# Kernel tuning notes

Hardware: AMD Instinct MI355X
Metric: run time of the kernel (lower is better)

## Reference

```python
import jax, jax.numpy as jnp
import numpy as np
from jax import lax

H = 12  # num_heads (from init_kwargs)


def _orthogonal_landmarks(q, num_landmarks):
    # q: (B, N, D) already scaled. Faithful to torch loop: recursively pick the
    # point whose max |cos sim| to the already-selected landmarks is minimal.
    B, N, D = q.shape
    nrm = jnp.linalg.norm(q, axis=-1, keepdims=True)
    qk = q / jnp.maximum(nrm, 1e-12)
    bidx = jnp.arange(B)
    key = jax.random.key(42)
    idx0 = jax.random.randint(key, (B,), 0, N)
    cur = qk[bidx, idx0]                             # (B, D)
    # running max |cos sim|; selected rows pinned to 10 (as in torch code)
    max_sim = jnp.zeros((B, N), qk.dtype).at[bidx, idx0].set(10.0)

    def step(carry, _):
        max_sim, cur = carry
        cos = jnp.abs(jnp.einsum('bnd,bd->bn', qk, cur))
        max_sim = jnp.maximum(max_sim, cos)
        idx = jnp.argmin(max_sim, axis=-1)
        cur2 = qk[bidx, idx]
        max_sim = max_sim.at[bidx, idx].set(10.0)
        return (max_sim, cur2), idx

    (_, _), idxs = lax.scan(step, (max_sim, cur), None, length=num_landmarks - 1)
    all_idx = jnp.concatenate([idx0[None, :], idxs], axis=0).T  # (B, L)
    landmarks = q[bidx[:, None], all_idx]                        # unnormalized q rows
    return lax.stop_gradient(landmarks)


def _orthoformer(q, k, v, num_landmarks, num_frames):
    # q,k,v: (B*h, N, D);  N = F * P
    Bh, N, D = q.shape
    F = num_frames
    P = N // F
    sc = D ** (-0.25)
    q = q * sc
    k = k * sc
    lm = _orthogonal_landmarks(q, num_landmarks)                 # (Bh, L, D)
    kernel_1 = jax.nn.softmax(jnp.einsum('bnd,bld->bnl', q, lm), axis=-1)   # (Bh,N,L)
    k2 = jnp.einsum('bld,bnd->bln', lm, k).reshape(Bh, num_landmarks, F, P)
    kernel_2 = jax.nn.softmax(k2, axis=-1)                       # (Bh,L,F,P)
    vr = v.reshape(Bh, F, P, D)
    x = jnp.einsum('blfp,bfpd->blfd', kernel_2, vr)
    x = jnp.einsum('bnl,blfd->bnfd', kernel_1, x)                # (Bh,N,F,D)
    return x


def setup_inputs() -> dict:
    key = jax.random.key(0)
    ks = jax.random.split(key, 6)
    B, F, P, C = 2, 16, 196, 768
    N = F * P
    s = 0.02
    x = jax.random.normal(ks[0], (B, N, C), jnp.float32)
    W_qkv = jax.random.normal(ks[1], (C, 3 * C), jnp.float32) * s
    W_pq = jax.random.normal(ks[2], (C, C), jnp.float32) * s
    W_pkv = jax.random.normal(ks[3], (C, 2 * C), jnp.float32) * s
    W_proj = jax.random.normal(ks[4], (C, C), jnp.float32) * s
    b_proj = jnp.zeros((C,), jnp.float32)
    return {"x": x, "W_qkv": W_qkv, "W_pq": W_pq, "W_pkv": W_pkv,
            "W_proj": W_proj, "b_proj": b_proj,
            "seq_len": P, "num_frames": F, "num_landmarks": 128}


def reference(x, W_qkv, W_pq, W_pkv, W_proj, b_proj, seq_len, num_frames, num_landmarks):
    B, N, C = x.shape
    F, P, h = num_frames, seq_len, H
    d = C // h
    scale = d ** (-0.5)
    qkv = x @ W_qkv                                              # (B,N,3C)
    q, k, v = jnp.split(qkv, 3, axis=-1)
    def to_bh(t):  # b n (h d) -> (b h) n d
        return t.reshape(B, N, h, d).transpose(0, 2, 1, 3).reshape(B * h, N, d)
    q_, k_, v_ = to_bh(q), to_bh(k), to_bh(v)
    xo = _orthoformer(q_, k_, v_, num_landmarks, F)              # (B*h,N,F,d)
    # (b h) s f d -> b s f (h d)
    xo = xo.reshape(B, h, N, F, d).transpose(0, 2, 3, 1, 4).reshape(B, N, F, C)
    # diagonal over (frame-of-query g, frame-of-key f)
    xd = xo.reshape(B, F, P, F, C)
    xdiag = jnp.diagonal(xd, axis1=1, axis2=3)                   # (B,P,C,F)
    xdiag = jnp.moveaxis(xdiag, -1, 1).reshape(B, N, C)          # b (f p) d
    q2 = xdiag @ W_pq                                            # (B,N,C)
    k2, v2 = jnp.split(xo @ W_pkv, 2, axis=-1)                   # (B,N,F,C) each
    q2 = q2.reshape(B, N, h, d).transpose(0, 2, 1, 3) * scale    # (B,h,N,d)
    k2 = k2.reshape(B, N, F, h, d).transpose(0, 3, 1, 2, 4)      # (B,h,N,F,d)
    v2 = v2.reshape(B, N, F, h, d).transpose(0, 3, 1, 2, 4)
    attn = jax.nn.softmax(jnp.einsum('bhsd,bhsfd->bhsf', q2, k2), axis=-1)
    out = jnp.einsum('bhsf,bhsfd->bhsd', attn, v2)               # (B,h,N,d)
    out = out.transpose(0, 2, 1, 3).reshape(B, N, C)
    out = out @ W_proj + b_proj
    return out, attn
```

## Files before the change

### kernel.cpp

```cpp
#include <hip/hip_runtime.h>


using u16 = unsigned short;
using u32 = unsigned int;
using u64 = unsigned long long;

typedef short bf16x8 __attribute__((ext_vector_type(8)));
typedef float f32x4 __attribute__((ext_vector_type(4)));

#define N_ 3136
#define C_ 768
#define H_ 12
#define F_ 16
#define P_ 196
#define L_ 128
#define SC_ 0.35355339059327373f
#define OUTPART_ ((size_t)2 * N_ * C_)
#define KB_ 8
#define RPB_ 392

__device__ __forceinline__ float b2f(u16 u) {
  u32 x = ((u32)u) << 16; float f; __builtin_memcpy(&f, &x, 4); return f;
}
__device__ __forceinline__ float lo16f(u32 u) {
  u32 x = u << 16; float f; __builtin_memcpy(&f, &x, 4); return f;
}
__device__ __forceinline__ float hi16f(u32 u) {
  u32 x = u & 0xFFFF0000u; float f; __builtin_memcpy(&f, &x, 4); return f;
}
__device__ __forceinline__ u16 f2b(float f) {
  u32 u; __builtin_memcpy(&u, &f, 4);
  u32 r = (u + 0x7FFFu + ((u >> 16) & 1u)) >> 16;
  return (u16)r;
}
__device__ __forceinline__ u64 d2u(double d) { u64 u; __builtin_memcpy(&u, &d, 8); return u; }

__device__ __forceinline__ void gll16(const void* g, void* l) {
  __builtin_amdgcn_global_load_lds(
      (__attribute__((address_space(1))) void*)g,
      (__attribute__((address_space(3))) void*)l, 16, 0, 0);
}

__global__ void detect_k(const u32* __restrict__ w, int* __restrict__ flag) {
  const int t = threadIdx.x;
  int hits = 0;
  #pragma unroll
  for (int i = 0; i < 16; ++i) {
    u32 word = w[t * 16 + i];
    u32 e = (word >> 7) & 0xFFu;
    if (e >= 110u && e <= 126u) hits++;
  }
  #pragma unroll
  for (int off = 32; off > 0; off >>= 1) hits += __shfl_down(hits, off);
  if (t == 0) flag[0] = (hits >= 512) ? 0 : 1;
}

__global__ void zcnt_k(u64* __restrict__ p) { if (threadIdx.x < 384) p[threadIdx.x] = 0ull; }

__device__ __forceinline__ void tf2(u32 k0, u32 k1v, u32 c0, u32 c1, u32& o0, u32& o1) {
  u32 ks[3] = {k0, k1v, k0 ^ k1v ^ 0x1BD11BDAu};
  u32 x0 = c0 + ks[0], x1 = c1 + ks[1];
  const u32 rA[4] = {13u, 15u, 26u, 6u}, rB[4] = {17u, 29u, 16u, 24u};
  #pragma unroll
  for (int r = 0; r < 5; ++r) {
    #pragma unroll
    for (int q = 0; q < 4; ++q) {
      u32 rot = (r & 1) ? rB[q] : rA[q];
      x0 += x1; x1 = (x1 << rot) | (x1 >> (32u - rot)); x1 ^= x0;
    }
    x0 += ks[(r + 1) % 3];
    x1 += ks[(r + 2) % 3] + (u32)(r + 1);
  }
  o0 = x0; o1 = x1;
}

__device__ __forceinline__ int tf_idx0(int bh) {
  u32 a0, a1, b0, b1;
  tf2(0u, 42u, 0u, 0u, a0, a1);
  tf2(0u, 42u, 0u, 1u, b0, b1);
  u32 j = (u32)bh;
  u32 h0, h1, l0, l1;
  tf2(a0, a1, 0u, j, h0, h1);
  u32 hi = h0 ^ h1;
  tf2(b0, b1, 0u, j, l0, l1);
  u32 lo = l0 ^ l1;
  return (int)(((hi % 3136u) * 2048u + (lo % 3136u)) % 3136u);
}

__global__ __launch_bounds__(256) void qselT_k(const void* __restrict__ xr, const void* __restrict__ wr,
                                               const int* __restrict__ flagp, float* __restrict__ qt)
{
  __shared__ float As[64 * 20];
  __shared__ float Bs[16 * 64];
  const int t = threadIdx.x;
  const int m0 = blockIdx.x * 64;
  const int n0 = blockIdx.y * 64;
  const int f32i = flagp[0];
  const int tx = t & 15, ty = t >> 4;
  float acc[4][4];
  #pragma unroll
  for (int i = 0; i < 4; ++i)
    #pragma unroll
    for (int j = 0; j < 4; ++j) acc[i][j] = 0.f;

  const int alr = t >> 2;
  const int alk = (t & 3) * 4;
  const int bkr = t >> 4;
  const int bnc = (t & 15) * 4;

  for (int k0 = 0; k0 < 768; k0 += 16) {
    float4 av, bv;
    if (f32i) {
      av = *(const float4*)((const float*)xr + (size_t)(m0 + alr) * 768 + k0 + alk);
      bv = *(const float4*)((const float*)wr + (size_t)(k0 + bkr) * 2304 + n0 + bnc);
    } else {
      const u16* xa = (const u16*)xr + (size_t)(m0 + alr) * 768 + k0 + alk;
      const u16* wa = (const u16*)wr + (size_t)(k0 + bkr) * 2304 + n0 + bnc;
      av.x = b2f(xa[0]); av.y = b2f(xa[1]); av.z = b2f(xa[2]); av.w = b2f(xa[3]);
      bv.x = b2f(wa[0]); bv.y = b2f(wa[1]); bv.z = b2f(wa[2]); bv.w = b2f(wa[3]);
    }
    As[alr * 20 + alk + 0] = av.x; As[alr * 20 + alk + 1] = av.y;
    As[alr * 20 + alk + 2] = av.z; As[alr * 20 + alk + 3] = av.w;
    *(float4*)(&Bs[bkr * 64 + bnc]) = bv;
    __syncthreads();
    #pragma unroll
    for (int kk = 0; kk < 16; ++kk) {
      float a[4], b[4];
      #pragma unroll
      for (int i = 0; i < 4; ++i) a[i] = As[(ty * 4 + i) * 20 + kk];
      #pragma unroll
      for (int j = 0; j < 4; ++j) b[j] = Bs[kk * 64 + tx * 4 + j];
      #pragma unroll
      for (int i = 0; i < 4; ++i)
        #pragma unroll
        for (int j = 0; j < 4; ++j) acc[i][j] += a[i] * b[j];
    }
    __syncthreads();
  }
  #pragma unroll
  for (int i = 0; i < 4; ++i) {
    const int m = m0 + ty * 4 + i;
    const int b = m / N_, n = m - b * N_;
    #pragma unroll
    for (int j = 0; j < 4; ++j) {
      const int col = n0 + tx * 4 + j;
      const int hh = col >> 6, dd = col & 63;
      qt[((size_t)(b * H_ + hh) * 64 + dd) * N_ + n] = acc[i][j] * SC_;
    }
  }
}

__global__ __launch_bounds__(512, 1) void landmarksR_k(
    const float* __restrict__ qt, float* __restrict__ lm, u64* __restrict__ cand)
{
  const int kb = blockIdx.x;
  const int bh = blockIdx.y;
  const float* QT = qt + (size_t)bh * 64 * N_;
  float* LM = lm + (size_t)bh * L_ * 64;
  u64* cd = cand + (size_t)bh * 16;
  __shared__ double curD[64];
  __shared__ u64 redV[8];
  __shared__ int redI[8];
  __shared__ int sW;
  const int t = threadIdx.x;
  const bool act = (t < RPB_);
  const int g = t >> 2, dc = t & 3, d0 = dc * 16;
  const int r0 = kb * RPB_;
  const int myRow = r0 + t;
  const float* base = QT + r0 + 4 * g;

  float4 qreg[16];
  #pragma unroll
  for (int i = 0; i < 16; ++i) qreg[i] = (float4){0.f, 0.f, 0.f, 0.f};
  if (act) {
    #pragma unroll
    for (int i = 0; i < 16; ++i) qreg[i] = *(const float4*)(base + (size_t)(d0 + i) * N_);
  }

  double inv_own = 0.0, ms_own = 0.0;
  if (act) {
    double s0 = 0.0, s1 = 0.0, s2 = 0.0, s3 = 0.0;
    #pragma unroll
    for (int i = 0; i < 16; ++i) {
      const float4 v = qreg[i];
      s0 += (double)v.x * (double)v.x; s1 += (double)v.y * (double)v.y;
      s2 += (double)v.z * (double)v.z; s3 += (double)v.w * (double)v.w;
    }
    s0 += __shfl_xor(s0, 1); s1 += __shfl_xor(s1, 1);
    s2 += __shfl_xor(s2, 1); s3 += __shfl_xor(s3, 1);
    s0 += __shfl_xor(s0, 2); s1 += __shfl_xor(s1, 2);
    s2 += __shfl_xor(s2, 2); s3 += __shfl_xor(s3, 2);
    const double sown = (dc == 0) ? s0 : (dc == 1) ? s1 : (dc == 2) ? s2 : s3;
    inv_own = 1.0 / fmax(sqrt(sown), 1e-12);
  }
  const int idx0 = tf_idx0(bh);
  if (act && myRow == idx0) ms_own = 10.0;

  if (t < 64) {
    const float vf = QT[(size_t)t * N_ + idx0];
    double v = (double)vf;
    double s = v * v;
    #pragma unroll
    for (int off = 32; off; off >>= 1) s += __shfl_xor(s, off);
    curD[t] = v / fmax(sqrt(s), 1e-12);
    if (kb == 0) LM[t] = vf;
  }
  __syncthreads();

  for (int step = 1; step < 128; ++step) {
    u64 bV = d2u(1e30); int bI = 0x7fffffff;
    if (act) {
      double a0 = 0.0, a1 = 0.0, a2 = 0.0, a3 = 0.0;
      #pragma unroll
      for (int i = 0; i < 16; ++i) {
        const float4 v = qreg[i];
        const double c = curD[d0 + i];
        a0 += (double)v.x * c; a1 += (double)v.y * c;
        a2 += (double)v.z * c; a3 += (double)v.w * c;
      }
      a0 += __shfl_xor(a0, 1); a1 += __shfl_xor(a1, 1);
      a2 += __shfl_xor(a2, 1); a3 += __shfl_xor(a3, 1);
      a0 += __shfl_xor(a0, 2); a1 += __shfl_xor(a1, 2);
      a2 += __shfl_xor(a2, 2); a3 += __shfl_xor(a3, 2);
      const double aown = (dc == 0) ? a0 : (dc == 1) ? a1 : (dc == 2) ? a2 : a3;
      ms_own = fmax(ms_own, fabs(aown * inv_own));
      bV = d2u(ms_own); bI = myRow;
    }
    #pragma unroll
    for (int off = 32; off; off >>= 1) {
      const u64 ov = __shfl_xor(bV, off);
      const int oi = __shfl_xor(bI, off);
      if (ov < bV || (ov == bV && oi < bI)) { bV = ov; bI = oi; }
    }
    if ((t & 63) == 0) { redV[t >> 6] = bV; redI[t >> 6] = bI; }
    __syncthreads();
    const int par = step & 1;
    if (t == 0) {
      u64 v = redV[0]; int ix = redI[0];
      #pragma unroll
      for (int w2 = 1; w2 < 8; ++w2)
        if (redV[w2] < v || (redV[w2] == v && redI[w2] < ix)) { v = redV[w2]; ix = redI[w2]; }
      const u64 pk = (v & ~((1ull << 19) - 1ull)) | ((u64)(u32)(step & 127) << 12) | (u64)(u32)ix;
      __hip_atomic_store(&cd[par * KB_ + kb], pk, __ATOMIC_RELAXED, __HIP_MEMORY_SCOPE_AGENT);
    }
    if (t < 64) {
      u64 pv = ~0ull;
      int ok = 1;
      for (;;) {
        if (t < KB_) {
          pv = __hip_atomic_load(&cd[par * KB_ + t], __ATOMIC_RELAXED, __HIP_MEMORY_SCOPE_AGENT);
          ok = ((int)((pv >> 12) & 127u) == step) ? 1 : 0;
        }
        if (__all(ok)) break;
        __builtin_amdgcn_s_sleep(1);
      }
      u64 m = (t < KB_) ? pv : ~0ull;
      #pragma unroll
      for (int off = 1; off < KB_; off <<= 1) {
        const u64 o = __shfl_xor(m, off);
        if (o < m) m = o;
      }
      if (t == 0) sW = (int)(m & 0xFFFu);
    }
    __syncthreads();
    const int w = sW;
    if (act && myRow == w) ms_own = 10.0;
    if (t < 64) {
      const float vf = QT[(size_t)t * N_ + w];
      double v = (double)vf;
      double s = v * v;
      #pragma unroll
      for (int off = 32; off; off >>= 1) s += __shfl_xor(s, off);
      curD[t] = v / fmax(sqrt(s), 1e-12);
      if (kb == 0) LM[(size_t)step * 64 + t] = vf;
    }
    __syncthreads();
  }
}

__global__ __launch_bounds__(256) void twT_k(const void* __restrict__ W, int K, int Nn,
                                             const int* __restrict__ flagp, u16* __restrict__ WT)
{
  __shared__ u16 Ts[64][80];
  const int t = threadIdx.x;
  const int k0 = blockIdx.x * 64, n0 = blockIdx.y * 64;
  const int f32i = flagp[0];
  const int kr = t >> 2, nc = (t & 3) * 16;
  u16 tmp[16];
  if (f32i) {
    const float* p = (const float*)W + (size_t)(k0 + kr) * Nn + n0 + nc;
    #pragma unroll
    for (int j = 0; j < 16; ++j) tmp[j] = f2b(p[j]);
  } else {
    const u16* p = (const u16*)W + (size_t)(k0 + kr) * Nn + n0 + nc;
    #pragma unroll
    for (int j = 0; j < 16; ++j) tmp[j] = p[j];
  }
  #pragma unroll
  for (int j = 0; j < 16; ++j) Ts[kr][nc + j] = tmp[j];
  __syncthreads();
  const int nr = t >> 2, kc = (t & 3) * 16;
  u16 o[16];
  #pragma unroll
  for (int j = 0; j < 16; ++j) o[j] = Ts[kc + j][nr];
  u16* dst = WT + (size_t)(n0 + nr) * K + k0 + kc;
  *(uint4*)(dst) = *(uint4*)(o);
  *(uint4*)(dst + 8) = *(uint4*)(o + 8);
}

__global__ __launch_bounds__(256) void xcvt_k(const void* __restrict__ x,
                                              const int* __restrict__ flagp, u16* __restrict__ xb)
{
  const int i = blockIdx.x * 256 + threadIdx.x;
  if (flagp[0]) {
    const float4* p = (const float4*)x + (size_t)i * 2;
    float4 f0 = p[0], f1 = p[1];
    u16 tmp[8] = { f2b(f0.x), f2b(f0.y), f2b(f0.z), f2b(f0.w),
                   f2b(f1.x), f2b(f1.y), f2b(f1.z), f2b(f1.w) };
    *(uint4*)(xb + (size_t)i * 8) = *(uint4*)tmp;
  } else {
    ((uint4*)xb)[i] = ((const uint4*)x)[i];
  }
}

template <int MODE>
__global__ __launch_bounds__(256) void gemm_k(
    const void* __restrict__ Ap, const void* __restrict__ Bp,
    int M, int K, int lda, int ldb, int n0c, int cn, const int* __restrict__ flagp,
    float* __restrict__ of0, u16* __restrict__ ob0, u16* __restrict__ ob1, u16* __restrict__ ob2,
    const void* __restrict__ biasRaw, void* __restrict__ outRaw)
{
  __shared__ u16 As[128 * 32];
  __shared__ u16 Bs[128 * 32];
  const int t = threadIdx.x;
  const int m0 = blockIdx.x * 128;
  const int n0 = blockIdx.y * 128;
  const int rf = (MODE == 4) ? flagp[0] : 0;

  size_t aOff = 0, bOff = 0;
  if constexpr (MODE == 1) {
    const int bh = blockIdx.z;
    aOff = (size_t)bh * ((size_t)N_ * 128) + (size_t)n0c * 128;
    bOff = (size_t)bh * (1024 * 128);
  }
  const int lane = t & 63;
  const int w = t >> 6;
  const int mw = (w >> 1) * 64;
  const int nw = (w & 1) * 64;
  const int lr = lane & 15;
  const int lk = lane >> 4;

  f32x4 acc[4][4];
  #pragma unroll
  for (int i = 0; i < 4; ++i)
    #pragma unroll
    for (int j = 0; j < 4; ++j) acc[i][j] = (f32x4){0.f, 0.f, 0.f, 0.f};

  const int c0 = w * 2, c1 = c0 + 1;
  const int rl = lane >> 2, sl = lane & 3;
  const int rowA0 = c0 * 16 + rl, rowA1 = c1 * 16 + rl;
  const int segA0 = (sl ^ ((rowA0 ^ (rowA0 >> 2)) & 3)) * 8;
  const int segA1 = (sl ^ ((rowA1 ^ (rowA1 >> 2)) & 3)) * 8;
  int ga0 = m0 + rowA0; if (ga0 >= M) ga0 = M - 1;
  int ga1 = m0 + rowA1; if (ga1 >= M) ga1 = M - 1;
  const u16* A16 = (const u16*)Ap;
  const u16* B16 = (const u16*)Bp;
  const u16* aP0 = A16 + aOff + (size_t)ga0 * lda + segA0;
  const u16* aP1 = A16 + aOff + (size_t)ga1 * lda + segA1;
  const u16* bP0 = B16 + bOff + (size_t)(n0 + rowA0) * ldb + segA0;
  const u16* bP1 = B16 + bOff + (size_t)(n0 + rowA1) * ldb + segA1;
  u16* lA0 = &As[c0 * 512]; u16* lA1 = &As[c1 * 512];
  u16* lB0 = &Bs[c0 * 512]; u16* lB1 = &Bs[c1 * 512];

  int roA[4], roB[4];
  #pragma unroll
  for (int q = 0; q < 4; ++q) {
    const int ra = mw + q * 16 + lr;
    roA[q] = ra * 32 + ((lk ^ ((ra ^ (ra >> 2)) & 3)) * 8);
    const int rb = nw + q * 16 + lr;
    roB[q] = rb * 32 + ((lk ^ ((rb ^ (rb >> 2)) & 3)) * 8);
  }

  for (int k0 = 0; k0 < K; k0 += 32) {
    gll16(aP0 + k0, lA0);
    gll16(aP1 + k0, lA1);
    gll16(bP0 + k0, lB0);
    gll16(bP1 + k0, lB1);
    __syncthreads();

    bf16x8 af[4], bfv[4];
    #pragma unroll
    for (int mt = 0; mt < 4; ++mt) af[mt] = *(const bf16x8*)(&As[roA[mt]]);
    #pragma unroll
    for (int nt = 0; nt < 4; ++nt) bfv[nt] = *(const bf16x8*)(&Bs[roB[nt]]);
    #pragma unroll
    for (int mt = 0; mt < 4; ++mt)
      #pragma unroll
      for (int nt = 0; nt < 4; ++nt)
        acc[mt][nt] = __builtin_amdgcn_mfma_f32_16x16x32_bf16(af[mt], bfv[nt], acc[mt][nt], 0, 0, 0);
    __syncthreads();
  }

  #pragma unroll
  for (int mt = 0; mt < 4; ++mt) {
    #pragma unroll
    for (int nt = 0; nt < 4; ++nt) {
      #pragma unroll
      for (int r = 0; r < 4; ++r) {
        const int grow = m0 + mw + mt * 16 + lk * 4 + r;
        const int gcol = n0 + nw + nt * 16 + lr;
        if (grow >= M) continue;
        float vv = acc[mt][nt][r];
        if constexpr (MODE == 0) {
          int b = (grow >= N_) ? 1 : 0;
          int n = grow - b * N_;
          int t3 = gcol / C_, cc = gcol - t3 * C_;
          int hh = cc >> 6, dd = cc & 63;
          size_t dst = (((size_t)(b * H_ + hh)) * N_ + n) * 64 + dd;
          if (t3 == 0) ob0[dst] = f2b(vv * SC_);
          else if (t3 == 1) ob1[dst] = f2b(vv * SC_);
          else ob2[dst] = f2b(vv);
        } else if constexpr (MODE == 1) {
          const int bh = blockIdx.z;
          int b = bh / H_, hh = bh - b * H_;
          int f = gcol >> 6, dd = gcol & 63;
          u16 wv = f2b(vv);
          ob0[(((size_t)(b * cn + grow)) * F_ + f) * C_ + hh * 64 + dd] = wv;
          int n = n0c + grow;
          if (f == n / P_) ob1[((size_t)(b * cn + grow)) * C_ + hh * 64 + dd] = wv;
        } else if constexpr (MODE == 2) {
          const int cn16 = cn * F_;
          int b = (grow >= cn16) ? 1 : 0;
          int r2 = grow - b * cn16;
          int ln = r2 >> 4, f = r2 & 15;
          int t2 = (gcol >= C_) ? 1 : 0, cc = gcol - t2 * C_;
          int hh = cc >> 6, dd = cc & 63;
          size_t dst = ((((size_t)(b * H_ + hh)) * cn + ln) * F_ + f) * 64 + dd;
          if (t2) ob1[dst] = f2b(vv); else ob0[dst] = f2b(vv);
        } else if constexpr (MODE == 3) {
          int b = (grow >= cn) ? 1 : 0;
          int ln = grow - b * cn;
          int hh = gcol >> 6, dd = gcol & 63;
          of0[(((size_t)(b * H_ + hh)) * cn + ln) * 64 + dd] = vv * 0.125f;
        } else {
          float bvad = rf ? ((const float*)biasRaw)[gcol] : b2f(((const u16*)biasRaw)[gcol]);
          float ov = vv + bvad;
          if (rf) ((float*)outRaw)[(size_t)grow * C_ + gcol] = ov;
          else    ((u16*)outRaw)[(size_t)grow * C_ + gcol] = f2b(ov);
        }
      }
    }
  }
}

__global__ __launch_bounds__(256) void k1_k(const u16* __restrict__ qb,
                                            const float* __restrict__ lm,
                                            u16* __restrict__ k1)
{
  const int bh = blockIdx.y;
  const int r0 = blockIdx.x * 64;
  __shared__ float qT[64][65];
  __shared__ float lmS[128 * 64];
  __shared__ float redA[4][64];
  __shared__ float redB[64];
  const int t = threadIdx.x;
  const u16* Q = qb + ((size_t)bh * N_ + r0) * 64;
  const float* Lm = lm + (size_t)bh * L_ * 64;
  for (int u = t; u < 2048; u += 256) ((float4*)lmS)[u] = ((const float4*)Lm)[u];
  for (int u = t; u < 512; u += 256) {
    int row = u >> 3, j0 = (u & 7) * 8;
    uint4 pk = *(const uint4*)(Q + (size_t)row * 64 + j0);
    const u16* pu = (const u16*)&pk;
    #pragma unroll
    for (int jj = 0; jj < 8; ++jj) qT[j0 + jj][row] = b2f(pu[jj]);
  }
  __syncthreads();
  const int row = t & 63, ch = t >> 6;
  float qr[64];
  #pragma unroll
  for (int j = 0; j < 64; ++j) qr[j] = qT[j][row];
  float s[32];
  for (int li = 0; li < 32; ++li) {
    const float* lp = lmS + (ch * 32 + li) * 64;
    float a = 0.f;
    #pragma unroll
    for (int j = 0; j < 64; ++j) a += lp[j] * qr[j];
    s[li] = a;
  }
  float mx = -1e30f;
  for (int li = 0; li < 32; ++li) mx = fmaxf(mx, s[li]);
  redA[ch][row] = mx;
  __syncthreads();
  if (t < 64) redB[t] = fmaxf(fmaxf(redA[0][t], redA[1][t]), fmaxf(redA[2][t], redA[3][t]));
  __syncthreads();
  mx = redB[row];
  float sum = 0.f;
  for (int li = 0; li < 32; ++li) { float e = __expf(s[li] - mx); s[li] = e; sum += e; }
  __syncthreads();
  redA[ch][row] = sum;
  __syncthreads();
  if (t < 64) redB[t] = 1.0f / (redA[0][t] + redA[1][t] + redA[2][t] + redA[3][t]);
  __syncthreads();
  const float inv = redB[row];
  u16* out = k1 + ((size_t)bh * N_ + r0 + row) * 128 + ch * 32;
  for (int li = 0; li < 32; ++li) out[li] = f2b(s[li] * inv);
}

__global__ __launch_bounds__(256) void k2x1_k(const float* __restrict__ lm,
                                              const u16* __restrict__ kb,
                                              const u16* __restrict__ vb,
                                              u16* __restrict__ x1)
{
  const int bh = blockIdx.x;
  const int f = blockIdx.y;
  __shared__ u16 kS[P_ * 64];
  __shared__ u16 vS[P_ * 64];
  __shared__ float redM[2][128];
  __shared__ float redS[2][128];
  const int t = threadIdx.x;
  const u16* Kf = kb + ((size_t)bh * N_ + f * P_) * 64;
  const u16* Vf = vb + ((size_t)bh * N_ + f * P_) * 64;
  for (int u = t; u < 1568; u += 256) {
    ((uint4*)kS)[u] = ((const uint4*)Kf)[u];
    ((uint4*)vS)[u] = ((const uint4*)Vf)[u];
  }
  __syncthreads();
  const int l = t & 127, half = t >> 7;
  const float* lp = lm + ((size_t)bh * L_ + l) * 64;
  float lr[64];
  #pragma unroll
  for (int j = 0; j < 64; ++j) lr[j] = lp[j];

  const int p0 = half * 98, p1 = p0 + 98;
  float mx = -1e30f;
  for (int p = p0; p < p1; ++p) {
    const uint4* kp = (const uint4*)(kS + p * 64);
    float s = 0.f;
    #pragma unroll
    for (int q4 = 0; q4 < 8; ++q4) {
      uint4 pk = kp[q4];
      const u32* pu = (const u32*)&pk;
      #pragma unroll
      for (int j2 = 0; j2 < 4; ++j2) {
        u32 u = pu[j2];
        s += lr[q4 * 8 + j2 * 2] * lo16f(u) + lr[q4 * 8 + j2 * 2 + 1] * hi16f(u);
      }
    }
    mx = fmaxf(mx, s);
  }
  redM[half][l] = mx;
  __syncthreads();
  mx = fmaxf(redM[0][l], redM[1][l]);

  float sm = 0.f;
  for (int p = p0; p < p1; ++p) {
    const uint4* kp = (const uint4*)(kS + p * 64);
    float s = 0.f;
    #pragma unroll
    for (int q4 = 0; q4 < 8; ++q4) {
      uint4 pk = kp[q4];
      const u32* pu = (const u32*)&pk;
      #pragma unroll
      for (int j2 = 0; j2 < 4; ++j2) {
        u32 u = pu[j2];
        s += lr[q4 * 8 + j2 * 2] * lo16f(u) + lr[q4 * 8 + j2 * 2 + 1] * hi16f(u);
      }
    }
    sm += __expf(s - mx);
  }
  redS[half][l] = sm;
  __syncthreads();
  const float inv = 1.0f / (redS[0][l] + redS[1][l]);

  const int dd0 = half * 32;
  float acc[32];
  #pragma unroll
  for (int u = 0; u < 32; ++u) acc[u] = 0.f;
  for (int p = 0; p < P_; ++p) {
    const uint4* kp = (const uint4*)(kS + p * 64);
    float s = 0.f;
    #pragma unroll
    for (int q4 = 0; q4 < 8; ++q4) {
      uint4 pk = kp[q4];
      const u32* pu = (const u32*)&pk;
      #pragma unroll
      for (int j2 = 0; j2 < 4; ++j2) {
        u32 u = pu[j2];
        s += lr[q4 * 8 + j2 * 2] * lo16f(u) + lr[q4 * 8 + j2 * 2 + 1] * hi16f(u);
      }
    }
    const float e = __expf(s - mx);
    const uint4* vp = (const uint4*)(vS + p * 64 + dd0);
    #pragma unroll
    for (int q4 = 0; q4 < 4; ++q4) {
      uint4 pv = vp[q4];
      const u32* pu = (const u32*)&pv;
      #pragma unroll
      for (int j2 = 0; j2 < 4; ++j2) {
        u32 u = pu[j2];
        acc[q4 * 8 + j2 * 2]     += e * lo16f(u);
        acc[q4 * 8 + j2 * 2 + 1] += e * hi16f(u);
      }
    }
  }
  u16* outT = x1 + (size_t)bh * (1024 * 128) + (size_t)(f * 64 + dd0) * 128 + l;
  for (int u = 0; u < 32; ++u) outT[(size_t)u * 128] = f2b(acc[u] * inv);
}

__global__ __launch_bounds__(256) void attn_k(const float* __restrict__ q2c,
                                              const u16* __restrict__ k2c,
                                              const u16* __restrict__ v2c,
                                              int n0c, int cn, const int* __restrict__ flagp,
                                              void* __restrict__ outRaw,
                                              u16* __restrict__ o)
{
  const int bh = blockIdx.y;
  const int b = bh / H_, hh = bh - b * H_;
  const int t = threadIdx.x;
  const int f32o = flagp[0];
  __shared__ float aS[64][17];
  const int nl = t >> 2, qi = t & 3;
  const int ln = blockIdx.x * 64 + nl;
  const bool act = ln < cn;
  const int n = n0c + ln;
  float q[64];
  if (act) {
    const float* qr = q2c + ((size_t)bh * cn + ln) * 64;
    #pragma unroll
    for (int j = 0; j < 64; ++j) q[j] = qr[j];
    float lg[4];
    #pragma unroll
    for (int ff = 0; ff < 4; ++ff) {
      const int f = qi * 4 + ff;
      const u16* kp = k2c + (((size_t)bh * cn + ln) * F_ + f) * 64;
      float s = 0.f;
      #pragma unroll
      for (int j8 = 0; j8 < 8; ++j8) {
        uint4 pk = ((const uint4*)kp)[j8];
        const u16* pu = (const u16*)&pk;
        #pragma unroll
        for (int u = 0; u < 8; ++u) s += q[j8 * 8 + u] * b2f(pu[u]);
      }
      lg[ff] = s;
    }
    float mx = fmaxf(fmaxf(lg[0], lg[1]), fmaxf(lg[2], lg[3]));
    mx = fmaxf(mx, __shfl_xor(mx, 1));
    mx = fmaxf(mx, __shfl_xor(mx, 2));
    float e[4], sm = 0.f;
    #pragma unroll
    for (int ff = 0; ff < 4; ++ff) { e[ff] = __expf(lg[ff] - mx); sm += e[ff]; }
    sm += __shfl_xor(sm, 1);
    sm += __shfl_xor(sm, 2);
    const float iv = 1.0f / sm;
    const size_t abase = ((size_t)bh * N_ + n) * F_ + qi * 4;
    #pragma unroll
    for (int ff = 0; ff < 4; ++ff) {
      const float a = e[ff] * iv;
      if (f32o) ((float*)outRaw)[OUTPART_ + abase + ff] = a;
      else      ((u16*)outRaw)[OUTPART_ + abase + ff] = f2b(a);
      aS[nl][qi * 4 + ff] = a;
    }
  }
  __syncthreads();
  if (act) {
    const int dd0 = qi * 16;
    float acc[16];
    #pragma unroll
    for (int u = 0; u < 16; ++u) acc[u] = 0.f;
    for (int f = 0; f < F_; ++f) {
      const float w2 = aS[nl][f];
      const u16* vp = v2c + (((size_t)bh * cn + ln) * F_ + f) * 64 + dd0;
      uint4 pv0 = ((const uint4*)vp)[0], pv1 = ((const uint4*)vp)[1];
      const u16* pu0 = (const u16*)&pv0;
      const u16* pu1 = (const u16*)&pv1;
      #pragma unroll
      for (int u = 0; u < 8; ++u) acc[u] += w2 * b2f(pu0[u]);
      #pragma unroll
      for (int u = 0; u < 8; ++u) acc[8 + u] += w2 * b2f(pu1[u]);
    }
    u16* op = o + ((size_t)(b * N_ + n)) * C_ + hh * 64 + dd0;
    for (int u = 0; u < 16; ++u) op[u] = f2b(acc[u]);
  }
}

extern "C" void kernel_launch(void* const* d_in, const int* in_sizes, int n_in,
                              void* d_out, int out_size, void* d_ws, size_t ws_size,
                              hipStream_t stream)
{
  (void)in_sizes; (void)n_in; (void)out_size;
  const void* x     = d_in[0];
  const void* Wqkv  = d_in[1];
  const void* Wpq   = d_in[2];
  const void* Wpkv  = d_in[3];
  const void* Wproj = d_in[4];
  const void* bproj = d_in[5];

  char* ws = (char*)d_ws;
  size_t off = 0;
  auto alloc = [&](size_t bytes) { void* p = ws + off; off += (bytes + 255) & ~(size_t)255; return p; };
  int*  flagp = (int*)alloc(256);
  u16*  qb  = (u16*)alloc(9633792);
  u16*  kb  = (u16*)alloc(9633792);
  u16*  vb  = (u16*)alloc(9633792);
  float* lm = (float*)alloc(786432);
  u16*  x1b = (u16*)alloc(6291456);
  u16*  ob  = (u16*)alloc(9633792);
  const size_t k1off = off;
  u16*  k1b = (u16*)alloc(19267584);
  const size_t chunk0 = off;

  const size_t qtNeed = k1off + 19267584 + 256;

  int Nc = 0;
  {
    const int cands[5] = {3136, 1568, 784, 392, 196};
    for (int i = 0; i < 5; ++i) {
      size_t need = chunk0 + (size_t)156672 * cands[i] + 1024;
      if (need <= ws_size && qtNeed <= ws_size) { Nc = cands[i]; break; }
    }
  }
  if (Nc == 0) return;
  const int nchunks = N_ / Nc;
  u16*  xoc = (u16*)(ws + chunk0);
  u16*  k2c = xoc + (size_t)24576 * Nc;
  u16*  v2c = k2c + (size_t)24576 * Nc;
  u16*  xdc = v2c + (size_t)24576 * Nc;
  float* q2c = (float*)(xdc + (size_t)1536 * Nc);
  float* qt  = (float*)(ws + k1off);

  u16* WqkvT = (u16*)(ws + k1off);
  u16* xb    = (u16*)(ws + k1off + 3538944);
  u16* WpkvT = kb;
  u16* WpqT  = kb + 1179648;
  u16* WprojT= kb + 1179648 + 589824;

  u64* cand = (u64*)(ws + chunk0);

  detect_k<<<1, 64, 0, stream>>>((const u32*)Wqkv, flagp);
  zcnt_k<<<1, 512, 0, stream>>>(cand);

  qselT_k<<<dim3(98, 12), 256, 0, stream>>>(x, Wqkv, flagp, qt);
  landmarksR_k<<<dim3(KB_, 24), 512, 0, stream>>>(qt, lm, cand);

  twT_k<<<dim3(12, 36), 256, 0, stream>>>(Wqkv, 768, 2304, flagp, WqkvT);
  xcvt_k<<<2352, 256, 0, stream>>>(x, flagp, xb);

  gemm_k<0><<<dim3(49, 18, 1), 256, 0, stream>>>(xb, WqkvT, 6272, 768, 768, 768, 0, 0, flagp,
                                                 nullptr, qb, kb, vb, nullptr, nullptr);
  k2x1_k<<<dim3(24, 16), 256, 0, stream>>>(lm, kb, vb, x1b);
  k1_k<<<dim3(49, 24), 256, 0, stream>>>(qb, lm, k1b);

  twT_k<<<dim3(12, 24), 256, 0, stream>>>(Wpkv, 768, 1536, flagp, WpkvT);
  twT_k<<<dim3(12, 12), 256, 0, stream>>>(Wpq, 768, 768, flagp, WpqT);
  twT_k<<<dim3(12, 12), 256, 0, stream>>>(Wproj, 768, 768, flagp, WprojT);

  for (int c = 0; c < nchunks; ++c) {
    const int n0c = c * Nc;
    gemm_k<1><<<dim3((Nc + 127) / 128, 8, 24), 256, 0, stream>>>(
        k1b, x1b, Nc, 128, 128, 128, n0c, Nc, flagp, nullptr, xoc, xdc, nullptr, nullptr, nullptr);
    gemm_k<2><<<dim3((2 * Nc * 16) / 128, 12, 1), 256, 0, stream>>>(
        xoc, WpkvT, 2 * Nc * 16, 768, 768, 768, n0c, Nc, flagp, nullptr, k2c, v2c, nullptr, nullptr, nullptr);
    gemm_k<3><<<dim3((2 * Nc + 127) / 128, 6, 1), 256, 0, stream>>>(
        xdc, WpqT, 2 * Nc, 768, 768, 768, n0c, Nc, flagp, q2c, nullptr, nullptr, nullptr, nullptr, nullptr);
    attn_k<<<dim3((Nc + 63) / 64, 24), 256, 0, stream>>>(
        q2c, k2c, v2c, n0c, Nc, flagp, d_out, ob);
  }
  gemm_k<4><<<dim3(49, 6, 1), 256, 0, stream>>>(ob, WprojT, 6272, 768, 768, 768, 0, 0, flagp,
                                                nullptr, nullptr, nullptr, nullptr, bproj, d_out);
}
```

Measured before the change: 1.770 ms.

## Merge weight transposes and post-projection GEMMs into fewer launches, retile qsel

Measured after the change: 1.658 ms. 6.3% less time.

```diff
diff --git a/kernel.cpp b/kernel.cpp
--- a/kernel.cpp
+++ b/kernel.cpp
@@ -90,56 +90,62 @@
 __global__ __launch_bounds__(256) void qselT_k(const void* __restrict__ xr, const void* __restrict__ wr,
                                                const int* __restrict__ flagp, float* __restrict__ qt)
 {
-  __shared__ float As[64 * 20];
+  __shared__ float As[128 * 20];
   __shared__ float Bs[16 * 64];
   const int t = threadIdx.x;
-  const int m0 = blockIdx.x * 64;
+  const int m0 = blockIdx.x * 128;
   const int n0 = blockIdx.y * 64;
   const int f32i = flagp[0];
   const int tx = t & 15, ty = t >> 4;
-  float acc[4][4];
-  #pragma unroll
-  for (int i = 0; i < 4; ++i)
+  float acc[8][4];
+  #pragma unroll
+  for (int i = 0; i < 8; ++i)
     #pragma unroll
     for (int j = 0; j < 4; ++j) acc[i][j] = 0.f;
 
-  const int alr = t >> 2;
-  const int alk = (t & 3) * 4;
+  const int alr = t >> 1;
+  const int alk = (t & 1) * 8;
   const int bkr = t >> 4;
   const int bnc = (t & 15) * 4;
 
   for (int k0 = 0; k0 < 768; k0 += 16) {
-    float4 av, bv;
+    float av[8];
+    float4 bv;
     if (f32i) {
-      av = *(const float4*)((const float*)xr + (size_t)(m0 + alr) * 768 + k0 + alk);
+      const float* xa = (const float*)xr + (size_t)(m0 + alr) * 768 + k0 + alk;
+      float4 a0 = *(const float4*)(xa);
+      float4 a1 = *(const float4*)(xa + 4);
+      av[0] = a0.x; av[1] = a0.y; av[2] = a0.z; av[3] = a0.w;
+      av[4] = a1.x; av[5] = a1.y; av[6] = a1.z; av[7] = a1.w;
       bv = *(const float4*)((const float*)wr + (size_t)(k0 + bkr) * 2304 + n0 + bnc);
     } else {
       const u16* xa = (const u16*)xr + (size_t)(m0 + alr) * 768 + k0 + alk;
+      #pragma unroll
+      for (int j = 0; j < 8; ++j) av[j] = b2f(xa[j]);
       const u16* wa = (const u16*)wr + (size_t)(k0 + bkr) * 2304 + n0 + bnc;
-      av.x = b2f(xa[0]); av.y = b2f(xa[1]); av.z = b2f(xa[2]); av.w = b2f(xa[3]);
       bv.x = b2f(wa[0]); bv.y = b2f(wa[1]); bv.z = b2f(wa[2]); bv.w = b2f(wa[3]);
     }
-    As[alr * 20 + alk + 0] = av.x; As[alr * 20 + alk + 1] = av.y;
-    As[alr * 20 + alk + 2] = av.z; As[alr * 20 + alk + 3] = av.w;
+    #pragma unroll
+    for (int j = 0; j < 8; ++j) As[alr * 20 + alk + j] = av[j];
     *(float4*)(&Bs[bkr * 64 + bnc]) = bv;
     __syncthreads();
     #pragma unroll
     for (int kk = 0; kk < 16; ++kk) {
-      float a[4], b[4];
-      #pragma unroll
-      for (int i = 0; i < 4; ++i) a[i] = As[(ty * 4 + i) * 20 + kk];
+      float a[8], b[4];
+      #pragma unroll
+      for (int i = 0; i < 8; ++i) a[i] = As[(ty * 8 + i) * 20 + kk];
       #pragma unroll
       for (int j = 0; j < 4; ++j) b[j] = Bs[kk * 64 + tx * 4 + j];
       #pragma unroll
-      for (int i = 0; i < 4; ++i)
+      for (int i = 0; i < 8; ++i)
         #pragma unroll
         for (int j = 0; j < 4; ++j) acc[i][j] += a[i] * b[j];
     }
     __syncthreads();
   }
   #pragma unroll
-  for (int i = 0; i < 4; ++i) {
-    const int m = m0 + ty * 4 + i;
+  for (int i = 0; i < 8; ++i) {
+    const int m = m0 + ty * 8 + i;
     const int b = m / N_, n = m - b * N_;
     #pragma unroll
     for (int j = 0; j < 4; ++j) {
@@ -153,8 +159,8 @@
 __global__ __launch_bounds__(512, 1) void landmarksR_k(
     const float* __restrict__ qt, float* __restrict__ lm, u64* __restrict__ cand)
 {
-  const int kb = blockIdx.x;
-  const int bh = blockIdx.y;
+  const int kb = blockIdx.y;
+  const int bh = blockIdx.x;
   const float* QT = qt + (size_t)bh * 64 * N_;
   float* LM = lm + (size_t)bh * L_ * 64;
   u64* cd = cand + (size_t)bh * 16;
@@ -278,13 +284,9 @@
   }
 }
 
-__global__ __launch_bounds__(256) void twT_k(const void* __restrict__ W, int K, int Nn,
-                                             const int* __restrict__ flagp, u16* __restrict__ WT)
-{
-  __shared__ u16 Ts[64][80];
-  const int t = threadIdx.x;
-  const int k0 = blockIdx.x * 64, n0 = blockIdx.y * 64;
-  const int f32i = flagp[0];
+__device__ __forceinline__ void twT_body(const void* W, int K, int Nn, int f32i,
+                                         u16* WT, int k0, int n0, int t, u16 (&Ts)[64][80])
+{
   const int kr = t >> 2, nc = (t & 3) * 16;
   u16 tmp[16];
   if (f32i) {
@@ -306,6 +308,26 @@
   u16* dst = WT + (size_t)(n0 + nr) * K + k0 + kc;
   *(uint4*)(dst) = *(uint4*)(o);
   *(uint4*)(dst + 8) = *(uint4*)(o + 8);
+}
+
+__global__ __launch_bounds__(256) void twT_k(const void* __restrict__ W, int K, int Nn,
+                                             const int* __restrict__ flagp, u16* __restrict__ WT)
+{
+  __shared__ u16 Ts[64][80];
+  twT_body(W, K, Nn, flagp[0], WT, blockIdx.x * 64, blockIdx.y * 64, threadIdx.x, Ts);
+}
+
+__global__ __launch_bounds__(256) void twT3_k(const void* __restrict__ W0, const void* __restrict__ W1,
+                                              const void* __restrict__ W2, const int* __restrict__ flagp,
+                                              u16* __restrict__ T0, u16* __restrict__ T1, u16* __restrict__ T2)
+{
+  __shared__ u16 Ts[64][80];
+  const int z = blockIdx.z;
+  const void* W = (z == 0) ? W0 : (z == 1) ? W1 : W2;
+  u16* WT = (z == 0) ? T0 : (z == 1) ? T1 : T2;
+  const int Nn = (z == 0) ? 1536 : 768;
+  if (blockIdx.y * 64 >= Nn) return;
+  twT_body(W, 768, Nn, flagp[0], WT, blockIdx.x * 64, blockIdx.y * 64, threadIdx.x, Ts);
 }
 
 __global__ __launch_bounds__(256) void xcvt_k(const void* __restrict__ x,
@@ -323,39 +345,23 @@
   }
 }
 
-template <int MODE>
-__global__ __launch_bounds__(256) void gemm_k(
-    const void* __restrict__ Ap, const void* __restrict__ Bp,
-    int M, int K, int lda, int ldb, int n0c, int cn, const int* __restrict__ flagp,
-    float* __restrict__ of0, u16* __restrict__ ob0, u16* __restrict__ ob1, u16* __restrict__ ob2,
-    const void* __restrict__ biasRaw, void* __restrict__ outRaw)
-{
-  __shared__ u16 As[128 * 32];
-  __shared__ u16 Bs[128 * 32];
-  const int t = threadIdx.x;
-  const int m0 = blockIdx.x * 128;
-  const int n0 = blockIdx.y * 128;
-  const int rf = (MODE == 4) ? flagp[0] : 0;
-
-  size_t aOff = 0, bOff = 0;
-  if constexpr (MODE == 1) {
-    const int bh = blockIdx.z;
-    aOff = (size_t)bh * ((size_t)N_ * 128) + (size_t)n0c * 128;
-    bOff = (size_t)bh * (1024 * 128);
-  }
+struct GemmCore {
+  const u16 *aP0, *aP1, *bP0, *bP1;
+  u16 *lA0, *lA1, *lB0, *lB1;
+  int roA[4], roB[4];
+  int mw, nw, lr, lk;
+};
+
+__device__ __forceinline__ void gemm_core_init(GemmCore& gc, u16* As, u16* Bs,
+    const u16* A16, const u16* B16, size_t aOff, size_t bOff,
+    int m0, int n0, int lda, int ldb, int M, int t)
+{
   const int lane = t & 63;
   const int w = t >> 6;
-  const int mw = (w >> 1) * 64;
-  const int nw = (w & 1) * 64;
-  const int lr = lane & 15;
-  const int lk = lane >> 4;
-
-  f32x4 acc[4][4];
-  #pragma unroll
-  for (int i = 0; i < 4; ++i)
-    #pragma unroll
-    for (int j = 0; j < 4; ++j) acc[i][j] = (f32x4){0.f, 0.f, 0.f, 0.f};
-
+  gc.mw = (w >> 1) * 64;
+  gc.nw = (w & 1) * 64;
+  gc.lr = lane & 15;
+  gc.lk = lane >> 4;
   const int c0 = w * 2, c1 = c0 + 1;
   const int rl = lane >> 2, sl = lane & 3;
   const int rowA0 = c0 * 16 + rl, rowA1 = c1 * 16 + rl;
@@ -363,36 +369,35 @@
   const int segA1 = (sl ^ ((rowA1 ^ (rowA1 >> 2)) & 3)) * 8;
   int ga0 = m0 + rowA0; if (ga0 >= M) ga0 = M - 1;
   int ga1 = m0 + rowA1; if (ga1 >= M) ga1 = M - 1;
-  const u16* A16 = (const u16*)Ap;
-  const u16* B16 = (const u16*)Bp;
-  const u16* aP0 = A16 + aOff + (size_t)ga0 * lda + segA0;
-  const u16* aP1 = A16 + aOff + (size_t)ga1 * lda + segA1;
-  const u16* bP0 = B16 + bOff + (size_t)(n0 + rowA0) * ldb + segA0;
-  const u16* bP1 = B16 + bOff + (size_t)(n0 + rowA1) * ldb + segA1;
-  u16* lA0 = &As[c0 * 512]; u16* lA1 = &As[c1 * 512];
-  u16* lB0 = &Bs[c0 * 512]; u16* lB1 = &Bs[c1 * 512];
-
-  int roA[4], roB[4];
+  gc.aP0 = A16 + aOff + (size_t)ga0 * lda + segA0;
+  gc.aP1 = A16 + aOff + (size_t)ga1 * lda + segA1;
+  gc.bP0 = B16 + bOff + (size_t)(n0 + rowA0) * ldb + segA0;
+  gc.bP1 = B16 + bOff + (size_t)(n0 + rowA1) * ldb + segA1;
+  gc.lA0 = &As[c0 * 512]; gc.lA1 = &As[c1 * 512];
+  gc.lB0 = &Bs[c0 * 512]; gc.lB1 = &Bs[c1 * 512];
   #pragma unroll
   for (int q = 0; q < 4; ++q) {
-    const int ra = mw + q * 16 + lr;
-    roA[q] = ra * 32 + ((lk ^ ((ra ^ (ra >> 2)) & 3)) * 8);
-    const int rb = nw + q * 16 + lr;
-    roB[q] = rb * 32 + ((lk ^ ((rb ^ (rb >> 2)) & 3)) * 8);
-  }
-
+    const int ra = gc.mw + q * 16 + gc.lr;
+    gc.roA[q] = ra * 32 + ((gc.lk ^ ((ra ^ (ra >> 2)) & 3)) * 8);
+    const int rb = gc.nw + q * 16 + gc.lr;
+    gc.roB[q] = rb * 32 + ((gc.lk ^ ((rb ^ (rb >> 2)) & 3)) * 8);
+  }
+}
+
+__device__ __forceinline__ void gemm_core_loop(const GemmCore& gc, u16* As, u16* Bs,
+                                               int K, f32x4 (&acc)[4][4])
+{
   for (int k0 = 0; k0 < K; k0 += 32) {
-    gll16(aP0 + k0, lA0);
-    gll16(aP1 + k0, lA1);
-    gll16(bP0 + k0, lB0);
-    gll16(bP1 + k0, lB1);
+    gll16(gc.aP0 + k0, gc.lA0);
+    gll16(gc.aP1 + k0, gc.lA1);
+    gll16(gc.bP0 + k0, gc.lB0);
+    gll16(gc.bP1 + k0, gc.lB1);
     __syncthreads();
-
     bf16x8 af[4], bfv[4];
     #pragma unroll
-    for (int mt = 0; mt < 4; ++mt) af[mt] = *(const bf16x8*)(&As[roA[mt]]);
-    #pragma unroll
-    for (int nt = 0; nt < 4; ++nt) bfv[nt] = *(const bf16x8*)(&Bs[roB[nt]]);
+    for (int mt = 0; mt < 4; ++mt) af[mt] = *(const bf16x8*)(&As[gc.roA[mt]]);
+    #pragma unroll
+    for (int nt = 0; nt < 4; ++nt) bfv[nt] = *(const bf16x8*)(&Bs[gc.roB[nt]]);
     #pragma unroll
     for (int mt = 0; mt < 4; ++mt)
       #pragma unroll
@@ -400,7 +405,39 @@
         acc[mt][nt] = __builtin_amdgcn_mfma_f32_16x16x32_bf16(af[mt], bfv[nt], acc[mt][nt], 0, 0, 0);
     __syncthreads();
   }
-
+}
+
+template <int MODE>
+__global__ __launch_bounds__(256) void gemm_k(
+    const void* __restrict__ Ap, const void* __restrict__ Bp,
+    int M, int K, int lda, int ldb, int n0c, int cn, const int* __restrict__ flagp,
+    float* __restrict__ of0, u16* __restrict__ ob0, u16* __restrict__ ob1, u16* __restrict__ ob2,
+    const void* __restrict__ biasRaw, void* __restrict__ outRaw)
+{
+  __shared__ u16 As[128 * 32];
+  __shared__ u16 Bs[128 * 32];
+  const int t = threadIdx.x;
+  const int m0 = blockIdx.x * 128;
+  const int n0 = blockIdx.y * 128;
+  const int rf = (MODE == 4) ? flagp[0] : 0;
+
+  size_t aOff = 0, bOff = 0;
+  if constexpr (MODE == 1) {
+    const int bh = blockIdx.z;
+    aOff = (size_t)bh * ((size_t)N_ * 128) + (size_t)n0c * 128;
+    bOff = (size_t)bh * (1024 * 128);
+  }
+  f32x4 acc[4][4];
+  #pragma unroll
+  for (int i = 0; i < 4; ++i)
+    #pragma unroll
+    for (int j = 0; j < 4; ++j) acc[i][j] = (f32x4){0.f, 0.f, 0.f, 0.f};
+
+  GemmCore gc;
+  gemm_core_init(gc, As, Bs, (const u16*)Ap, (const u16*)Bp, aOff, bOff, m0, n0, lda, ldb, M, t);
+  gemm_core_loop(gc, As, Bs, K, acc);
+
+  const int lr = gc.lr, lk = gc.lk, mw = gc.mw, nw = gc.nw;
   #pragma unroll
   for (int mt = 0; mt < 4; ++mt) {
     #pragma unroll
@@ -428,7 +465,56 @@
           ob0[(((size_t)(b * cn + grow)) * F_ + f) * C_ + hh * 64 + dd] = wv;
           int n = n0c + grow;
           if (f == n / P_) ob1[((size_t)(b * cn + grow)) * C_ + hh * 64 + dd] = wv;
-        } else if constexpr (MODE == 2) {
+        } else {
+          float bvad = rf ? ((const float*)biasRaw)[gcol] : b2f(((const u16*)biasRaw)[gcol]);
+          float ov = vv + bvad;
+          if (rf) ((float*)outRaw)[(size_t)grow * C_ + gcol] = ov;
+          else    ((u16*)outRaw)[(size_t)grow * C_ + gcol] = f2b(ov);
+        }
+      }
+    }
+  }
+}
+
+__global__ __launch_bounds__(256) void gemm23_k(
+    const u16* __restrict__ xoc, const u16* __restrict__ xdc,
+    const u16* __restrict__ WpkvT, const u16* __restrict__ WpqT,
+    int cn, float* __restrict__ q2c, u16* __restrict__ k2c, u16* __restrict__ v2c)
+{
+  __shared__ u16 As[128 * 32];
+  __shared__ u16 Bs[128 * 32];
+  const int t = threadIdx.x;
+  const int z = blockIdx.z;
+  const int m0 = blockIdx.x * 128;
+  const int n0 = blockIdx.y * 128;
+  const int M = z ? (2 * cn) : (2 * cn * F_);
+  const int NN = z ? 768 : 1536;
+  if (m0 >= M || n0 >= NN) return;
+  const u16* Ap = z ? xdc : xoc;
+  const u16* Bp = z ? WpqT : WpkvT;
+
+  f32x4 acc[4][4];
+  #pragma unroll
+  for (int i = 0; i < 4; ++i)
+    #pragma unroll
+    for (int j = 0; j < 4; ++j) acc[i][j] = (f32x4){0.f, 0.f, 0.f, 0.f};
+
+  GemmCore gc;
+  gemm_core_init(gc, As, Bs, Ap, Bp, 0, 0, m0, n0, 768, 768, M, t);
+  gemm_core_loop(gc, As, Bs, 768, acc);
+
+  const int lr = gc.lr, lk = gc.lk, mw = gc.mw, nw = gc.nw;
+  #pragma unroll
+  for (int mt = 0; mt < 4; ++mt) {
+    #pragma unroll
+    for (int nt = 0; nt < 4; ++nt) {
+      #pragma unroll
+      for (int r = 0; r < 4; ++r) {
+        const int grow = m0 + mw + mt * 16 + lk * 4 + r;
+        const int gcol = n0 + nw + nt * 16 + lr;
+        if (grow >= M) continue;
+        float vv = acc[mt][nt][r];
+        if (z == 0) {
           const int cn16 = cn * F_;
           int b = (grow >= cn16) ? 1 : 0;
           int r2 = grow - b * cn16;
@@ -436,17 +522,12 @@
           int t2 = (gcol >= C_) ? 1 : 0, cc = gcol - t2 * C_;
           int hh = cc >> 6, dd = cc & 63;
           size_t dst = ((((size_t)(b * H_ + hh)) * cn + ln) * F_ + f) * 64 + dd;
-          if (t2) ob1[dst] = f2b(vv); else ob0[dst] = f2b(vv);
-        } else if constexpr (MODE == 3) {
+          if (t2) v2c[dst] = f2b(vv); else k2c[dst] = f2b(vv);
+        } else {
           int b = (grow >= cn) ? 1 : 0;
           int ln = grow - b * cn;
           int hh = gcol >> 6, dd = gcol & 63;
-          of0[(((size_t)(b * H_ + hh)) * cn + ln) * 64 + dd] = vv * 0.125f;
-        } else {
-          float bvad = rf ? ((const float*)biasRaw)[gcol] : b2f(((const u16*)biasRaw)[gcol]);
-          float ov = vv + bvad;
-          if (rf) ((float*)outRaw)[(size_t)grow * C_ + gcol] = ov;
-          else    ((u16*)outRaw)[(size_t)grow * C_ + gcol] = f2b(ov);
+          q2c[(((size_t)(b * H_ + hh)) * cn + ln) * 64 + dd] = vv * 0.125f;
         }
       }
     }
@@ -739,8 +820,8 @@
   detect_k<<<1, 64, 0, stream>>>((const u32*)Wqkv, flagp);
   zcnt_k<<<1, 512, 0, stream>>>(cand);
 
-  qselT_k<<<dim3(98, 12), 256, 0, stream>>>(x, Wqkv, flagp, qt);
-  landmarksR_k<<<dim3(KB_, 24), 512, 0, stream>>>(qt, lm, cand);
+  qselT_k<<<dim3(49, 12), 256, 0, stream>>>(x, Wqkv, flagp, qt);
+  landmarksR_k<<<dim3(24, KB_), 512, 0, stream>>>(qt, lm, cand);
 
   twT_k<<<dim3(12, 36), 256, 0, stream>>>(Wqkv, 768, 2304, flagp, WqkvT);
   xcvt_k<<<2352, 256, 0, stream>>>(x, flagp, xb);
@@ -750,18 +831,14 @@
   k2x1_k<<<dim3(24, 16), 256, 0, stream>>>(lm, kb, vb, x1b);
   k1_k<<<dim3(49, 24), 256, 0, stream>>>(qb, lm, k1b);
 
-  twT_k<<<dim3(12, 24), 256, 0, stream>>>(Wpkv, 768, 1536, flagp, WpkvT);
-  twT_k<<<dim3(12, 12), 256, 0, stream>>>(Wpq, 768, 768, flagp, WpqT);
-  twT_k<<<dim3(12, 12), 256, 0, stream>>>(Wproj, 768, 768, flagp, WprojT);
+  twT3_k<<<dim3(12, 24, 3), 256, 0, stream>>>(Wpkv, Wpq, Wproj, flagp, WpkvT, WpqT, WprojT);
 
   for (int c = 0; c < nchunks; ++c) {
     const int n0c = c * Nc;
     gemm_k<1><<<dim3((Nc + 127) / 128, 8, 24), 256, 0, stream>>>(
         k1b, x1b, Nc, 128, 128, 128, n0c, Nc, flagp, nullptr, xoc, xdc, nullptr, nullptr, nullptr);
-    gemm_k<2><<<dim3((2 * Nc * 16) / 128, 12, 1), 256, 0, stream>>>(
-        xoc, WpkvT, 2 * Nc * 16, 768, 768, 768, n0c, Nc, flagp, nullptr, k2c, v2c, nullptr, nullptr, nullptr);
-    gemm_k<3><<<dim3((2 * Nc + 127) / 128, 6, 1), 256, 0, stream>>>(
-        xdc, WpqT, 2 * Nc, 768, 768, 768, n0c, Nc, flagp, q2c, nullptr, nullptr, nullptr, nullptr, nullptr);
+    gemm23_k<<<dim3(Nc / 4, 12, 2), 256, 0, stream>>>(
+        xoc, xdc, WpkvT, WpqT, Nc, q2c, k2c, v2c);
     attn_k<<<dim3((Nc + 63) / 64, 24), 256, 0, stream>>>(
         q2c, k2c, v2c, n0c, Nc, flagp, d_out, ob);
   }
```
